# Optimization experiments

Hardware: AMD Instinct MI355X
Metric: run time of the kernel (lower is better)

The kernel has to match this reference:

```python
import math
import jax, jax.numpy as jnp
import numpy as np

DIM = 4096
N_HEADS = 32
N_KV_HEADS = 8
HEAD_DIM = DIM // N_HEADS        # 128
N_REP = N_HEADS // N_KV_HEADS    # 4
BSZ = 1
SEQ = 2048
ROPE_THETA = 500000.0


def setup_inputs() -> dict:
    key = jax.random.key(0)
    ks = jax.random.split(key, 5)
    scale = 1.0 / math.sqrt(DIM)
    x = jax.random.normal(ks[0], (BSZ, SEQ, DIM), dtype=jnp.float32)
    wq = jax.random.normal(ks[1], (N_HEADS * HEAD_DIM, DIM), dtype=jnp.float32) * scale
    wk = jax.random.normal(ks[2], (N_KV_HEADS * HEAD_DIM, DIM), dtype=jnp.float32) * scale
    wv = jax.random.normal(ks[3], (N_KV_HEADS * HEAD_DIM, DIM), dtype=jnp.float32) * scale
    wo = jax.random.normal(ks[4], (N_HEADS * HEAD_DIM, DIM), dtype=jnp.float32).T * scale
    wo = jnp.asarray(wo)  # [DIM, N_HEADS*HEAD_DIM] like nn.Linear(in=heads*hd, out=dim).weight
    # RoPE tables: freqs_cis[t, j] = exp(i * t * theta^{-2j/head_dim}), j in [0, head_dim/2)
    inv_freq = 1.0 / (ROPE_THETA ** (np.arange(0, HEAD_DIM, 2, dtype=np.float32) / HEAD_DIM))
    t = np.arange(SEQ, dtype=np.float32)
    ang = np.outer(t, inv_freq)  # [SEQ, HEAD_DIM//2]
    freqs_cos = jnp.asarray(np.cos(ang), dtype=jnp.float32)
    freqs_sin = jnp.asarray(np.sin(ang), dtype=jnp.float32)
    # additive causal mask [SEQ, SEQ]
    mask = jnp.where(jnp.tril(jnp.ones((SEQ, SEQ), dtype=bool)), 0.0, -1e9).astype(jnp.float32)
    return {"x": x, "wq": wq, "wk": wk, "wv": wv, "wo": wo,
            "freqs_cos": freqs_cos, "freqs_sin": freqs_sin, "mask": mask}


def _apply_rope(xh, cos, sin):
    # xh: [b, s, h, head_dim]; cos/sin: [s, head_dim//2]
    b, s, h, d = xh.shape
    xr = xh.reshape(b, s, h, d // 2, 2)
    x0, x1 = xr[..., 0], xr[..., 1]
    c = cos[None, :, None, :]
    sn = sin[None, :, None, :]
    o0 = x0 * c - x1 * sn
    o1 = x0 * sn + x1 * c
    return jnp.stack([o0, o1], axis=-1).reshape(b, s, h, d)


def reference(x, wq, wk, wv, wo, freqs_cos, freqs_sin, mask):
    bsz, seqlen, _ = x.shape
    xq = (x @ wq.T).reshape(bsz, seqlen, N_HEADS, HEAD_DIM)
    xk = (x @ wk.T).reshape(bsz, seqlen, N_KV_HEADS, HEAD_DIM)
    xv = (x @ wv.T).reshape(bsz, seqlen, N_KV_HEADS, HEAD_DIM)
    xq = _apply_rope(xq, freqs_cos, freqs_sin)
    xk = _apply_rope(xk, freqs_cos, freqs_sin)
    # repeat_kv (GQA expansion)
    keys = jnp.repeat(xk, N_REP, axis=2)    # [b, s, N_HEADS, hd]
    values = jnp.repeat(xv, N_REP, axis=2)
    scores = jnp.einsum('bqhd,bkhd->bhqk', xq, keys) / math.sqrt(HEAD_DIM)
    scores = scores + mask[None, None, :, :]
    scores = jax.nn.softmax(scores.astype(jnp.float32), axis=-1).astype(xq.dtype)
    out = jnp.einsum('bhqk,bkhd->bqhd', scores, values)
    out = out.reshape(bsz, seqlen, N_HEADS * HEAD_DIM)
    return out @ wo.T
```

## Files before the change

### kernel.cpp

```cpp
#include <hip/hip_runtime.h>
#include <math.h>
#include <stdint.h>
#include <stddef.h>


typedef __attribute__((ext_vector_type(8))) short bf16x8;
typedef __attribute__((ext_vector_type(4))) short bf16x4;
typedef __attribute__((ext_vector_type(4))) float f32x4;
typedef unsigned short u16;
typedef unsigned int u32;

#define NEG_BIG (-1.0e9f)
#define MFMA32(a, b, c) __builtin_amdgcn_mfma_f32_16x16x32_bf16(a, b, c, 0, 0, 0)
#define SFENCE() __builtin_amdgcn_sched_barrier(0)
#define BAR() __builtin_amdgcn_s_barrier()
#define VMW(n_) asm volatile("s_waitcnt vmcnt(" #n_ ")" ::: "memory")

__device__ __forceinline__ float bf2f(u16 b) {
    return __uint_as_float(((unsigned int)b) << 16);
}
__device__ __forceinline__ u16 f2bf(float f) {
    unsigned int u = __float_as_uint(f);
    u += 0x7fff + ((u >> 16) & 1);
    return (u16)(u >> 16);
}
__device__ __forceinline__ void gld_lds16(short* lds, const u16* g) {
    __builtin_amdgcn_global_load_lds(
        (const __attribute__((address_space(1))) void*)g,
        (__attribute__((address_space(3))) void*)lds, 16, 0, 0);
}
__device__ __forceinline__ void cvt8(const float* __restrict__ s,
                                     u16* __restrict__ d, int i) {
    float4 a, c;
    __builtin_memcpy(&a, s + i, 16);
    __builtin_memcpy(&c, s + i + 4, 16);
    bf16x8 o;
    o[0] = (short)f2bf(a.x); o[1] = (short)f2bf(a.y);
    o[2] = (short)f2bf(a.z); o[3] = (short)f2bf(a.w);
    o[4] = (short)f2bf(c.x); o[5] = (short)f2bf(c.y);
    o[6] = (short)f2bf(c.z); o[7] = (short)f2bf(c.w);
    __builtin_memcpy(d + i, &o, 16);
}

__global__ __launch_bounds__(256) void cvt_all(
    const float* __restrict__ x, const float* __restrict__ wq,
    const float* __restrict__ wk, const float* __restrict__ wv,
    u16* __restrict__ xb, u16* __restrict__ wqb, u16* __restrict__ wkb,
    u16* __restrict__ wvb) {
    const int b = blockIdx.x;
    const float* s; u16* d; int off;
    if (b < 4096)       { s = x;  d = xb;  off = b; }
    else if (b < 12288) { s = wq; d = wqb; off = b - 4096; }
    else if (b < 14336) { s = wk; d = wkb; off = b - 12288; }
    else                { s = wv; d = wvb; off = b - 14336; }
    cvt8(s, d, off * 2048 + threadIdx.x * 8);
}


#define QSTGA(bf_, ks_, kt_)                                                 \
    { _Pragma("unroll") for (int r_ = 0; r_ < 2; ++r_)                       \
        gld_lds16(Ad + (bf_) * 16384 + (ks_) * 8192 + r_ * 4096,             \
                  Ag + gK * r_ + (size_t)(kt_) * 64 + (ks_) * 32); }
#define QSTGB(bf_, ks_, kt_)                                                 \
    { _Pragma("unroll") for (int r_ = 0; r_ < 2; ++r_)                       \
        gld_lds16(Bd + (bf_) * 16384 + (ks_) * 8192 + r_ * 4096,             \
                  Bg + gK * r_ + (size_t)(kt_) * 64 + (ks_) * 32); }
#define QRDA(bank_, bf_, ks_, mh_)                                           \
    { _Pragma("unroll") for (int i_ = 0; i_ < 4; ++i_)                       \
        __builtin_memcpy(&bank_[i_], S + (bf_) * 16384 + (ks_) * 8192 +      \
                         abase + ((mh_) * 64 + i_ * 16) * 32, 16); }
#define QRDB(bank_, bf_, ks_)                                                \
    { _Pragma("unroll") for (int n_ = 0; n_ < 4; ++n_)                       \
        __builtin_memcpy(&bank_[n_], Bs + (bf_) * 16384 + (ks_) * 8192 +     \
                         bbase + n_ * 512, 16); }
#define QMM(afb_, bfb_, mh_)                                                 \
    {                                                                        \
        __builtin_amdgcn_s_setprio(1);                                       \
        _Pragma("unroll") for (int i_ = 0; i_ < 4; ++i_)                     \
            _Pragma("unroll") for (int n_ = 0; n_ < 4; ++n_)                 \
                acc[(mh_) * 4 + i_][n_] =                                    \
                    MFMA32(afb_[i_], bfb_[n_], acc[(mh_) * 4 + i_][n_]);     \
        __builtin_amdgcn_s_setprio(0);                                       \
    }

template <int OUT, int ROPE>
__device__ __forceinline__ void gemm_q(const u16* __restrict__ A,
                                       const u16* __restrict__ B,
                                       void* __restrict__ C,
                                       const float* __restrict__ fc,
                                       const float* __restrict__ fs,
                                       int mb, int nb, int N, int K,
                                       short* __restrict__ S) {
    short* const Bs = S + 32768;
    const int t = threadIdx.x;
    const int lane = t & 63, l15 = lane & 15, quad = lane >> 4;
    const int wid = t >> 6, wr = wid >> 2, wc = wid & 3;

    const int srow = t >> 2;
    const int cs = (t & 3) ^ ((t >> 3) & 3);
    const u16* const Ag = A + (size_t)(mb * 256 + srow) * K + cs * 8;
    const u16* const Bg = B + (size_t)(nb * 256 + srow) * K + cs * 8;
    short* const Ad = S + t * 8;
    short* const Bd = Bs + t * 8;
    const size_t gK = (size_t)128 * K;

    const int swz = (quad ^ ((l15 >> 1) & 3)) * 8;
    const int abase = (wr * 128 + l15) * 32 + swz;
    const int bbase = (wc * 64 + l15) * 32 + swz;

    f32x4 acc[8][4] = {};
    bf16x8 af0[4], af1[4], bf0[4], bf1[4];

    QSTGA(0, 0, 0); QSTGB(0, 0, 0);
    QSTGA(0, 1, 0); QSTGB(0, 1, 0);
    QSTGA(1, 0, 1); QSTGB(1, 0, 1);
    VMW(8);
    BAR();
    QRDA(af0, 0, 0, 0); QRDB(bf0, 0, 0);
    SFENCE();

    const int nIt = K >> 7;
    for (int it = 0; it < nIt - 1; ++it) {
        const int k1 = 2 * it + 1, kn0 = 2 * it + 2, kn1 = 2 * it + 3;
        QSTGA(1, 1, k1);  QRDA(af1, 0, 0, 1);                    QMM(af0, bf0, 0); SFENCE(); VMW(6); BAR();
        QSTGB(1, 1, k1);  QRDA(af0, 0, 1, 0); QRDB(bf1, 0, 1);   QMM(af1, bf0, 1); SFENCE();         BAR();
        QSTGA(0, 0, kn0); QRDA(af1, 0, 1, 1);                    QMM(af0, bf1, 0); SFENCE(); VMW(6); BAR();
        QSTGB(0, 0, kn0); QRDA(af0, 1, 0, 0); QRDB(bf0, 1, 0);   QMM(af1, bf1, 1); SFENCE();         BAR();
        QSTGA(0, 1, kn0); QRDA(af1, 1, 0, 1);                    QMM(af0, bf0, 0); SFENCE(); VMW(6); BAR();
        QSTGB(0, 1, kn0); QRDA(af0, 1, 1, 0); QRDB(bf1, 1, 1);   QMM(af1, bf0, 1); SFENCE();         BAR();
        QSTGA(1, 0, kn1); QRDA(af1, 1, 1, 1);                    QMM(af0, bf1, 0); SFENCE(); VMW(6); BAR();
        QSTGB(1, 0, kn1); QRDA(af0, 0, 0, 0); QRDB(bf0, 0, 0);   QMM(af1, bf1, 1); SFENCE();         BAR();
    }
    {
        const int k1 = 2 * nIt - 1;
        QSTGA(1, 1, k1);  QRDA(af1, 0, 0, 1);                    QMM(af0, bf0, 0); SFENCE(); VMW(6); BAR();
        QSTGB(1, 1, k1);  QRDA(af0, 0, 1, 0); QRDB(bf1, 0, 1);   QMM(af1, bf0, 1); SFENCE();         BAR();
        QRDA(af1, 0, 1, 1);                                      QMM(af0, bf1, 0); SFENCE(); VMW(4); BAR();
        QRDA(af0, 1, 0, 0); QRDB(bf0, 1, 0);                     QMM(af1, bf1, 1); SFENCE();         BAR();
        QRDA(af1, 1, 0, 1);                                      QMM(af0, bf0, 0); SFENCE(); VMW(0); BAR();
        QRDA(af0, 1, 1, 0); QRDB(bf1, 1, 1);                     QMM(af1, bf0, 1); SFENCE();         BAR();
        QRDA(af1, 1, 1, 1);                                      QMM(af0, bf1, 0); SFENCE();         BAR();
        QMM(af1, bf1, 1);
    }

#pragma unroll
    for (int i8 = 0; i8 < 8; ++i8) {
        const int rowb = mb * 256 + wr * 128 + (i8 >> 2) * 64 +
                         (i8 & 3) * 16 + quad * 4;
#pragma unroll
        for (int j = 0; j < 4; ++j) {
            const int col = nb * 256 + wc * 64 + j * 16 + l15;
            if (OUT == 2) {
                bf16x4 v;
#pragma unroll
                for (int r = 0; r < 4; ++r) v[r] = (short)f2bf(acc[i8][j][r]);
                __builtin_memcpy((u16*)C + (size_t)col * 2048 + rowb, &v, 8);
            } else if (ROPE) {
                const int pi = (col & 127) >> 1;
                const bool odd = (l15 & 1);
#pragma unroll
                for (int r = 0; r < 4; ++r) {
                    const int s = rowb + r;
                    const float c = fc[s * 64 + pi];
                    const float sn = fs[s * 64 + pi];
                    const float v = acc[i8][j][r];
                    const float vp = __shfl_xor(v, 1);
                    const float out = odd ? (vp * sn + v * c)
                                          : (v * c - vp * sn);
                    ((u16*)C)[(size_t)s * N + col] = f2bf(out);
                }
            } else {
#pragma unroll
                for (int r = 0; r < 4; ++r)
                    ((u16*)C)[(size_t)(rowb + r) * N + col] =
                        f2bf(acc[i8][j][r]);
            }
        }
    }
}

__global__ __launch_bounds__(512, 2) void qkv_proj8(
    const u16* __restrict__ x,
    const u16* __restrict__ wq, const u16* __restrict__ wk,
    const u16* __restrict__ wv,
    const float* __restrict__ wof, u16* __restrict__ wob,
    const float* __restrict__ fc, const float* __restrict__ fs,
    u16* __restrict__ Q, u16* __restrict__ Kc, u16* __restrict__ Vt) {
    __shared__ __align__(16) short S[65536];
    const int lid = blockIdx.x;
    if (lid >= 192) {
        const int cb = lid - 192, t = threadIdx.x;
        for (int it = 0; it < 64; ++it)
            cvt8(wof, wob, ((cb * 64 + it) * 512 + t) * 8);
        return;
    }
    const int swzb = (lid & 7) * 24 + (lid >> 3);
    const int mb = swzb & 7, y = swzb >> 3;
    if (y < 16)
        gemm_q<0, 1>(x, wq, Q, fc, fs, mb, y, 4096, 4096, S);
    else if (y < 20)
        gemm_q<0, 1>(x, wk, Kc, fc, fs, mb, y - 16, 1024, 4096, S);
    else
        gemm_q<2, 0>(x, wv, Vt, fc, fs, mb, y - 20, 1024, 4096, S);
}


#define O8_STG(bf_, ks_, kt_)                                                \
    {                                                                        \
        gld_lds16(Ad + (bf_) * 8192 + (ks_) * 4096,                          \
                  Ag + (size_t)(kt_) * 64 + (ks_) * 32);                     \
        _Pragma("unroll") for (int r_ = 0; r_ < 2; ++r_)                     \
            gld_lds16(Bd + (bf_) * 16384 + (ks_) * 8192 + r_ * 4096,         \
                      Bg + gK * r_ + (size_t)(kt_) * 64 + (ks_) * 32);       \
    }
#define O8_PHASE(bf_, ks_, STAGE_, WAIT_)                                    \
    {                                                                        \
        _Pragma("unroll") for (int n_ = 0; n_ < 4; ++n_)                     \
            __builtin_memcpy(&bfr[n_], Bs + (bf_) * 16384 + (ks_) * 8192 +   \
                                           bbase + n_ * 512, 16);            \
        _Pragma("unroll") for (int i_ = 0; i_ < 4; ++i_)                     \
            __builtin_memcpy(&af[i_], S + (bf_) * 8192 + (ks_) * 4096 +      \
                                          abase + i_ * 512, 16);             \
        STAGE_;                                                              \
        SFENCE();                                                            \
        __builtin_amdgcn_s_barrier();                                        \
        asm volatile("s_waitcnt lgkmcnt(0)" ::: "memory");                   \
        SFENCE();                                                            \
        __builtin_amdgcn_s_setprio(1);                                       \
        _Pragma("unroll") for (int i_ = 0; i_ < 4; ++i_)                     \
            _Pragma("unroll") for (int n_ = 0; n_ < 4; ++n_)                 \
                acc[i_][n_] = MFMA32(af[i_], bfr[n_], acc[i_][n_]);          \
        __builtin_amdgcn_s_setprio(0);                                       \
        SFENCE();                                                            \
        WAIT_;                                                               \
        __builtin_amdgcn_s_barrier();                                        \
    }

__global__ __launch_bounds__(512, 2) void oproj8(
    const u16* __restrict__ A, const u16* __restrict__ wo,
    float* __restrict__ out) {
    __shared__ __align__(16) short S[49152];
    short* const Bs = S + 16384;
    const int lid = blockIdx.x;
    const int logical = (lid & 7) * 32 + (lid >> 3);
    const int mb = logical & 15, nb = logical >> 4;

    const int t = threadIdx.x;
    const int lane = t & 63, l15 = lane & 15, quad = lane >> 4;
    const int wid = t >> 6, wr = wid >> 2, wc = wid & 3;

    const int srow = t >> 2;
    const int cs = (t & 3) ^ ((t >> 3) & 3);
    const u16* const Ag = A + (size_t)(mb * 128 + srow) * 4096 + cs * 8;
    const u16* const Bg = wo + (size_t)(nb * 256 + srow) * 4096 + cs * 8;
    short* const Ad = S + t * 8;
    short* const Bd = Bs + t * 8;
    const size_t gK = (size_t)128 * 4096;

    const int swz = (quad ^ ((l15 >> 1) & 3)) * 8;
    const int abase = (wr * 64 + l15) * 32 + swz;
    const int bbase = (wc * 64 + l15) * 32 + swz;

    f32x4 acc[4][4] = {};
    bf16x8 af[4], bfr[4];

    O8_STG(0, 0, 0); O8_STG(0, 1, 0); O8_STG(1, 0, 1);
    VMW(6);
    BAR();

    const int nIt = 32;
    for (int it = 0; it < nIt - 1; ++it) {
        const int k1 = 2 * it + 1, kn0 = 2 * it + 2, kn1 = 2 * it + 3;
        O8_PHASE(0, 0, O8_STG(1, 1, k1),  VMW(6));
        O8_PHASE(0, 1, O8_STG(0, 0, kn0), VMW(6));
        O8_PHASE(1, 0, O8_STG(0, 1, kn0), VMW(6));
        O8_PHASE(1, 1, O8_STG(1, 0, kn1), VMW(6));
    }
    {
        const int k1 = 2 * nIt - 1;
        O8_PHASE(0, 0, O8_STG(1, 1, k1), VMW(6));
        O8_PHASE(0, 1, ,                 VMW(3));
        O8_PHASE(1, 0, ,                 VMW(0));
        O8_PHASE(1, 1, , );
    }

#pragma unroll
    for (int i = 0; i < 4; ++i) {
        const int rowb = mb * 128 + wr * 64 + i * 16 + quad * 4;
#pragma unroll
        for (int j = 0; j < 4; ++j) {
            const int col = nb * 256 + wc * 64 + j * 16 + l15;
#pragma unroll
            for (int r = 0; r < 4; ++r)
                out[(size_t)(rowb + r) * 4096 + col] = acc[i][j][r];
        }
    }
}

__device__ __forceinline__ int kswz(int row, int cs) {
    int f = (row & 3) | ((row & 8) >> 1);
    return row * 128 + ((cs ^ f) << 3);
}

template <bool MASKED>
__device__ __forceinline__ void fa_step_lds(
    const short* __restrict__ Kl, const short* __restrict__ Vl,
    int kb, int kadd, int q0, int l15, int quad,
    const int (&koff)[8], const int (&voff)[8],
    const bf16x8 (&qf)[4], const bf16x8 vones,
    f32x4 (&o)[8], f32x4& o9, float& m) {
    const float c1 = 0.08838834764831845f * 1.4426950408889634f;

    bf16x8 kf[8];
#pragma unroll
    for (int i = 0; i < 8; ++i)
        __builtin_memcpy(&kf[i], Kl + koff[i] + kadd, 16);
    f32x4 s0 = {0, 0, 0, 0}, s1 = {0, 0, 0, 0};
#pragma unroll
    for (int c = 0; c < 4; ++c) {
        s0 = MFMA32(kf[c], qf[c], s0);
        s1 = MFMA32(kf[4 + c], qf[c], s1);
    }

    bf16x8 vf[8];
#pragma unroll
    for (int n = 0; n < 8; ++n) __builtin_memcpy(&vf[n], Vl + voff[n], 16);

    float sv0[4], sv1[4];
    const int q = q0 + l15;
#pragma unroll
    for (int r = 0; r < 4; ++r) {
        sv0[r] = s0[r];
        sv1[r] = s1[r];
        if (MASKED) {
            if (kb + 8 * quad + r > q) sv0[r] = NEG_BIG;
            if (kb + 8 * quad + 4 + r > q) sv1[r] = NEG_BIG;
        }
    }

    float mx = fmaxf(fmaxf(fmaxf(sv0[0], sv0[1]), fmaxf(sv0[2], sv0[3])),
                     fmaxf(fmaxf(sv1[0], sv1[1]), fmaxf(sv1[2], sv1[3])));
    mx = fmaxf(mx, __shfl_xor(mx, 16));
    mx = fmaxf(mx, __shfl_xor(mx, 32));

    if (!__all(mx <= m + 90.0f)) {
        float mnew = fmaxf(m, mx);
        float alpha = exp2f((m - mnew) * c1);
        float aO[4];
#pragma unroll
        for (int r = 0; r < 4; ++r) aO[r] = __shfl(alpha, quad * 20 + r);
#pragma unroll
        for (int n = 0; n < 8; ++n)
#pragma unroll
            for (int r = 0; r < 4; ++r) o[n][r] *= aO[r];
#pragma unroll
        for (int r = 0; r < 4; ++r) o9[r] *= aO[r];
        m = mnew;
    }

    const float mc = m * c1;
    float p0[4], p1[4];
#pragma unroll
    for (int r = 0; r < 4; ++r) {
        p0[r] = exp2f(__builtin_fmaf(sv0[r], c1, -mc));
        p1[r] = exp2f(__builtin_fmaf(sv1[r], c1, -mc));
    }

    u32 w0, w1, w2, w3;
    asm("v_cvt_pk_bf16_f32 %0, %1, %2" : "=v"(w0) : "v"(p0[0]), "v"(p0[1]));
    asm("v_cvt_pk_bf16_f32 %0, %1, %2" : "=v"(w1) : "v"(p0[2]), "v"(p0[3]));
    asm("v_cvt_pk_bf16_f32 %0, %1, %2" : "=v"(w2) : "v"(p1[0]), "v"(p1[1]));
    asm("v_cvt_pk_bf16_f32 %0, %1, %2" : "=v"(w3) : "v"(p1[2]), "v"(p1[3]));
    u32 wa[4] = {w0, w1, w2, w3};
    bf16x8 pa;
    __builtin_memcpy(&pa, wa, 16);

#pragma unroll
    for (int n = 0; n < 8; ++n) o[n] = MFMA32(pa, vf[n], o[n]);
    o9 = MFMA32(pa, vones, o9);
}

__device__ __forceinline__ void fa_task(
    const u16* __restrict__ Q, const u16* __restrict__ Kc,
    const u16* __restrict__ Vt, u16* __restrict__ O,
    short* __restrict__ Kl0, short* __restrict__ Vl0,
    int q0, int nbt64, int h, int kvh, int t) {
    const int lane = t & 63;
    const int l15 = lane & 15, quad = lane >> 4;

    bf16x8 qf[4];
    const u16* qp = Q + (size_t)(q0 + l15) * 4096 + h * 128 + quad * 8;
#pragma unroll
    for (int c = 0; c < 4; ++c) __builtin_memcpy(&qf[c], qp + c * 32, 16);

    bf16x8 vones;
#pragma unroll
    for (int i = 0; i < 8; ++i) vones[i] = (short)0x3F80;

    const u16* ksrc[4]; short* kdst[4];
    const u16* vsrc[4]; short* vdst[4];
#pragma unroll
    for (int r = 0; r < 4; ++r) {
        int row = (t >> 4) + 16 * r;
        int slot = t & 15;
        int f = (row & 3) | ((row & 8) >> 1);
        int cks = slot ^ f;
        ksrc[r] = Kc + (size_t)row * 1024 + kvh * 128 + cks * 8;
        kdst[r] = Kl0 + (t + 256 * r) * 8;
        int rowv = (t >> 3) + 32 * r;
        int csv = (t & 7) ^ ((t >> 3) & 7);
        vsrc[r] = Vt + (size_t)(kvh * 128 + rowv) * 2048 + csv * 8;
        vdst[r] = Vl0 + (t + 256 * r) * 8;
    }

    const int rk0 = 8 * (l15 >> 2) + (l15 & 3);
    int koff[8], voff0[8], voff1[8];
#pragma unroll
    for (int c = 0; c < 4; ++c) {
        koff[c] = kswz(rk0, quad + c * 4);
        koff[4 + c] = kswz(rk0 + 4, quad + c * 4);
    }
#pragma unroll
    for (int n = 0; n < 8; ++n) {
        const int row = n * 16 + l15;
        voff0[n] = row * 64 + ((quad ^ (l15 & 7)) << 3);
        voff1[n] = row * 64 + (((quad + 4) ^ (l15 & 7)) << 3);
    }

    f32x4 o[8] = {};
    f32x4 o9 = {0, 0, 0, 0};
    float m = NEG_BIG;
    const int my_nb32 = (q0 + 47) / 32;

#pragma unroll
    for (int r = 0; r < 4; ++r) {
        gld_lds16(kdst[r], ksrc[r]);
        gld_lds16(vdst[r], vsrc[r]);
    }
    __syncthreads();

    for (int ib = 0; ib < nbt64; ++ib) {
        if (ib + 1 < nbt64) {
            const int kb = (ib + 1) * 64;
            const int bo = ((ib + 1) & 1) * 8192;
#pragma unroll
            for (int r = 0; r < 4; ++r) {
                gld_lds16(kdst[r] + bo, ksrc[r] + (size_t)kb * 1024);
                gld_lds16(vdst[r] + bo, vsrc[r] + kb);
            }
        }
        const short* Kl = Kl0 + (ib & 1) * 8192;
        const short* Vl = Vl0 + (ib & 1) * 8192;
#pragma unroll
        for (int sub = 0; sub < 2; ++sub) {
            const int ib32 = 2 * ib + sub;
            if (ib32 < my_nb32) {
                const int kb = ib * 64 + sub * 32;
                const int kadd = sub * 4096;
                if (ib32 == my_nb32 - 1)
                    fa_step_lds<true>(Kl, Vl, kb, kadd, q0, l15, quad, koff,
                                      sub ? voff1 : voff0, qf, vones, o, o9,
                                      m);
                else
                    fa_step_lds<false>(Kl, Vl, kb, kadd, q0, l15, quad, koff,
                                       sub ? voff1 : voff0, qf, vones, o, o9,
                                       m);
            }
        }
        __syncthreads();
    }

    float inv[4];
#pragma unroll
    for (int r = 0; r < 4; ++r) inv[r] = 1.f / o9[r];
#pragma unroll
    for (int n = 0; n < 8; ++n)
#pragma unroll
        for (int r = 0; r < 4; ++r) {
            int row = q0 + quad * 4 + r;
            O[(size_t)row * 4096 + h * 128 + n * 16 + l15] =
                f2bf(o[n][r] * inv[r]);
        }
}

__global__ __launch_bounds__(256, 2) void flash_attn(
    const u16* __restrict__ Q, const u16* __restrict__ Kc,
    const u16* __restrict__ Vt, u16* __restrict__ O) {
    __shared__ __align__(16) short Kl[2 * 64 * 128];
    __shared__ __align__(16) short Vl[2 * 128 * 64];
    const int pp = blockIdx.x;
    const int h = blockIdx.y;
    const int kvh = h >> 2;
    const int t = threadIdx.x, wave = t >> 6;
    fa_task(Q, Kc, Vt, O, Kl, Vl, pp * 64 + wave * 16, pp + 1, h, kvh, t);
    const int tb = 31 - pp;
    fa_task(Q, Kc, Vt, O, Kl, Vl, tb * 64 + (3 - wave) * 16, tb + 1, h,
            kvh, t);
}

extern "C" void kernel_launch(void* const* d_in, const int* in_sizes, int n_in,
                              void* d_out, int out_size, void* d_ws,
                              size_t ws_size, hipStream_t stream) {
    const float* x  = (const float*)d_in[0];
    const float* wq = (const float*)d_in[1];
    const float* wk = (const float*)d_in[2];
    const float* wv = (const float*)d_in[3];
    const float* wo = (const float*)d_in[4];
    const float* fc = (const float*)d_in[5];
    const float* fs = (const float*)d_in[6];
    float* out = (float*)d_out;

    const int NX = 2048 * 4096;
    const int NQW = 4096 * 4096;
    const int NKW = 1024 * 4096;
    const int NKV = 2048 * 1024;

    u16* Q   = (u16*)d_ws;
    u16* Kc  = Q   + NX;
    u16* Vt  = Kc  + NKV;
    u16* Ao  = Vt  + NKV;
    u16* xb  = Ao  + NX;
    u16* wqb = xb  + NX;
    u16* wkb = wqb + NQW;
    u16* wvb = wkb + NKW;
    u16* wob = wvb + NKW;

    cvt_all<<<16384, 256, 0, stream>>>(x, wq, wk, wv, xb, wqb, wkb, wvb);
    qkv_proj8<<<256, 512, 0, stream>>>(xb, wqb, wkb, wvb, wo, wob, fc, fs,
                                       Q, Kc, Vt);
    flash_attn<<<dim3(16, 32), 256, 0, stream>>>(Q, Kc, Vt, Ao);
    oproj8<<<256, 512, 0, stream>>>(Ao, wob, out);
}
```

Baseline: 456.0 us.

## Use one q-tile per block with 32-key LDS stages and higher occupancy

Flash attention drops the paired causal q-tile scheme, where each block ran a short and a long tile. Each block now handles one 64-row query tile, launched in descending tile order across a 32x32 grid. K/V LDS staging shrinks to 32-key double-buffered stages, with a new V swizzle. Launch bounds move to 4 blocks per SM so occupancy can hide latency. The cost is load imbalance left to the hardware scheduler, plus twice as many barriers per key range.

New measurement: 476.3 us. +4.5%, slower.

```diff
diff --git a/kernel.cpp b/kernel.cpp
--- a/kernel.cpp
+++ b/kernel.cpp
@@ -305,7 +305,7 @@
 template <bool MASKED>
 __device__ __forceinline__ void fa_step_lds(
     const short* __restrict__ Kl, const short* __restrict__ Vl,
-    int kb, int kadd, int q0, int l15, int quad,
+    int kb, int q0, int l15, int quad,
     const int (&koff)[8], const int (&voff)[8],
     const bf16x8 (&qf)[4], const bf16x8 vones,
     f32x4 (&o)[8], f32x4& o9, float& m) {
@@ -313,8 +313,7 @@
 
     bf16x8 kf[8];
 #pragma unroll
-    for (int i = 0; i < 8; ++i)
-        __builtin_memcpy(&kf[i], Kl + koff[i] + kadd, 16);
+    for (int i = 0; i < 8; ++i) __builtin_memcpy(&kf[i], Kl + koff[i], 16);
     f32x4 s0 = {0, 0, 0, 0}, s1 = {0, 0, 0, 0};
 #pragma unroll
     for (int c = 0; c < 4; ++c) {
@@ -380,13 +379,17 @@
     o9 = MFMA32(pa, vones, o9);
 }
 
-__device__ __forceinline__ void fa_task(
+__global__ __launch_bounds__(256, 4) void flash_attn(
     const u16* __restrict__ Q, const u16* __restrict__ Kc,
-    const u16* __restrict__ Vt, u16* __restrict__ O,
-    short* __restrict__ Kl0, short* __restrict__ Vl0,
-    int q0, int nbt64, int h, int kvh, int t) {
-    const int lane = t & 63;
-    const int l15 = lane & 15, quad = lane >> 4;
+    const u16* __restrict__ Vt, u16* __restrict__ O) {
+    __shared__ __align__(16) short Kl[2 * 32 * 128];
+    __shared__ __align__(16) short Vl[2 * 128 * 32];
+    const int tb = 31 - blockIdx.x;
+    const int h = blockIdx.y;
+    const int kvh = h >> 2;
+    const int t = threadIdx.x, wave = t >> 6;
+    const int lane = t & 63, l15 = lane & 15, quad = lane >> 4;
+    const int q0 = tb * 64 + wave * 16;
 
     bf16x8 qf[4];
     const u16* qp = Q + (size_t)(q0 + l15) * 4096 + h * 128 + quad * 8;
@@ -397,75 +400,65 @@
 #pragma unroll
     for (int i = 0; i < 8; ++i) vones[i] = (short)0x3F80;
 
-    const u16* ksrc[4]; short* kdst[4];
-    const u16* vsrc[4]; short* vdst[4];
-#pragma unroll
-    for (int r = 0; r < 4; ++r) {
+    const u16* ksrc[2]; short* kdst[2];
+    const u16* vsrc[2]; short* vdst[2];
+#pragma unroll
+    for (int r = 0; r < 2; ++r) {
         int row = (t >> 4) + 16 * r;
         int slot = t & 15;
         int f = (row & 3) | ((row & 8) >> 1);
         int cks = slot ^ f;
         ksrc[r] = Kc + (size_t)row * 1024 + kvh * 128 + cks * 8;
-        kdst[r] = Kl0 + (t + 256 * r) * 8;
-        int rowv = (t >> 3) + 32 * r;
-        int csv = (t & 7) ^ ((t >> 3) & 7);
+        kdst[r] = Kl + (t + 256 * r) * 8;
+        int rowv = (t >> 2) + 64 * r;
+        int csv = (t & 3) ^ ((t >> 3) & 3);
         vsrc[r] = Vt + (size_t)(kvh * 128 + rowv) * 2048 + csv * 8;
-        vdst[r] = Vl0 + (t + 256 * r) * 8;
+        vdst[r] = Vl + (t + 256 * r) * 8;
     }
 
     const int rk0 = 8 * (l15 >> 2) + (l15 & 3);
-    int koff[8], voff0[8], voff1[8];
+    int koff[8], voff[8];
 #pragma unroll
     for (int c = 0; c < 4; ++c) {
         koff[c] = kswz(rk0, quad + c * 4);
         koff[4 + c] = kswz(rk0 + 4, quad + c * 4);
     }
-#pragma unroll
-    for (int n = 0; n < 8; ++n) {
-        const int row = n * 16 + l15;
-        voff0[n] = row * 64 + ((quad ^ (l15 & 7)) << 3);
-        voff1[n] = row * 64 + (((quad + 4) ^ (l15 & 7)) << 3);
-    }
+    const int vswz = (quad ^ ((l15 >> 1) & 3)) * 8;
+#pragma unroll
+    for (int n = 0; n < 8; ++n) voff[n] = (n * 16 + l15) * 32 + vswz;
 
     f32x4 o[8] = {};
     f32x4 o9 = {0, 0, 0, 0};
     float m = NEG_BIG;
-    const int my_nb32 = (q0 + 47) / 32;
-
-#pragma unroll
-    for (int r = 0; r < 4; ++r) {
-        gld_lds16(kdst[r], ksrc[r]);
-        gld_lds16(vdst[r], vsrc[r]);
+    const int nbt = 2 * tb + 2;
+    const int my_nb = (q0 + 47) / 32;
+
+    {
+        gld_lds16(kdst[0], ksrc[0]);
+        gld_lds16(kdst[1], ksrc[1]);
+        gld_lds16(vdst[0], vsrc[0]);
+        gld_lds16(vdst[1], vsrc[1]);
     }
     __syncthreads();
 
-    for (int ib = 0; ib < nbt64; ++ib) {
-        if (ib + 1 < nbt64) {
-            const int kb = (ib + 1) * 64;
-            const int bo = ((ib + 1) & 1) * 8192;
-#pragma unroll
-            for (int r = 0; r < 4; ++r) {
-                gld_lds16(kdst[r] + bo, ksrc[r] + (size_t)kb * 1024);
-                gld_lds16(vdst[r] + bo, vsrc[r] + kb);
-            }
+    for (int ib = 0; ib < nbt; ++ib) {
+        if (ib + 1 < nbt) {
+            int kb = (ib + 1) * 32;
+            int bo = ((ib + 1) & 1) * 4096;
+            gld_lds16(kdst[0] + bo, ksrc[0] + (size_t)kb * 1024);
+            gld_lds16(kdst[1] + bo, ksrc[1] + (size_t)kb * 1024);
+            gld_lds16(vdst[0] + bo, vsrc[0] + kb);
+            gld_lds16(vdst[1] + bo, vsrc[1] + kb);
         }
-        const short* Kl = Kl0 + (ib & 1) * 8192;
-        const short* Vl = Vl0 + (ib & 1) * 8192;
-#pragma unroll
-        for (int sub = 0; sub < 2; ++sub) {
-            const int ib32 = 2 * ib + sub;
-            if (ib32 < my_nb32) {
-                const int kb = ib * 64 + sub * 32;
-                const int kadd = sub * 4096;
-                if (ib32 == my_nb32 - 1)
-                    fa_step_lds<true>(Kl, Vl, kb, kadd, q0, l15, quad, koff,
-                                      sub ? voff1 : voff0, qf, vones, o, o9,
-                                      m);
-                else
-                    fa_step_lds<false>(Kl, Vl, kb, kadd, q0, l15, quad, koff,
-                                       sub ? voff1 : voff0, qf, vones, o, o9,
-                                       m);
-            }
+        if (ib < my_nb) {
+            const short* Klb = Kl + (ib & 1) * 4096;
+            const short* Vlb = Vl + (ib & 1) * 4096;
+            if (ib == my_nb - 1)
+                fa_step_lds<true>(Klb, Vlb, ib * 32, q0, l15, quad, koff,
+                                  voff, qf, vones, o, o9, m);
+            else
+                fa_step_lds<false>(Klb, Vlb, ib * 32, q0, l15, quad, koff,
+                                   voff, qf, vones, o, o9, m);
         }
         __syncthreads();
     }
@@ -481,21 +474,6 @@
             O[(size_t)row * 4096 + h * 128 + n * 16 + l15] =
                 f2bf(o[n][r] * inv[r]);
         }
-}
-
-__global__ __launch_bounds__(256, 2) void flash_attn(
-    const u16* __restrict__ Q, const u16* __restrict__ Kc,
-    const u16* __restrict__ Vt, u16* __restrict__ O) {
-    __shared__ __align__(16) short Kl[2 * 64 * 128];
-    __shared__ __align__(16) short Vl[2 * 128 * 64];
-    const int pp = blockIdx.x;
-    const int h = blockIdx.y;
-    const int kvh = h >> 2;
-    const int t = threadIdx.x, wave = t >> 6;
-    fa_task(Q, Kc, Vt, O, Kl, Vl, pp * 64 + wave * 16, pp + 1, h, kvh, t);
-    const int tb = 31 - pp;
-    fa_task(Q, Kc, Vt, O, Kl, Vl, tb * 64 + (3 - wave) * 16, tb + 1, h,
-            kvh, t);
 }
 
 extern "C" void kernel_launch(void* const* d_in, const int* in_sizes, int n_in,
@@ -528,6 +506,6 @@
     cvt_all<<<16384, 256, 0, stream>>>(x, wq, wk, wv, xb, wqb, wkb, wvb);
     qkv_proj8<<<256, 512, 0, stream>>>(xb, wqb, wkb, wvb, wo, wob, fc, fs,
                                        Q, Kc, Vt);
-    flash_attn<<<dim3(16, 32), 256, 0, stream>>>(Q, Kc, Vt, Ao);
+    flash_attn<<<dim3(32, 32), 256, 0, stream>>>(Q, Kc, Vt, Ao);
     oproj8<<<256, 512, 0, stream>>>(Ao, wob, out);
 }
```
